# Kernel tuning notes

Hardware: AMD Instinct MI355X
Metric: run time of the kernel (lower is better)

The kernel has to match this reference:

```python
import jax, jax.numpy as jnp
import numpy as np

B, S, P = 2, 1024, 1024          # batch, new tokens, start_pos (cached prefix)
E, H, KV, HD = 2048, 32, 8, 64    # embed, heads, kv groups, head_dim
G = H // KV                       # group size = 4
THETA = 500000.0
CTX = P + S                       # cache/context length = 2048


def _rope_tables(start, seqlen):
    inv_freq = 1.0 / (THETA ** (jnp.arange(0, HD, 2, dtype=jnp.float32) / HD))
    pos = jnp.arange(start, start + seqlen, dtype=jnp.float32)
    freqs = jnp.outer(pos, inv_freq)              # [S, HD/2]
    emb = jnp.concatenate([freqs, freqs], axis=-1)  # [S, HD]
    return jnp.cos(emb), jnp.sin(emb)


def setup_inputs() -> dict:
    key = jax.random.key(0)
    ks = jax.random.split(key, 8)
    x = jax.random.normal(ks[0], (B, S, E), dtype=jnp.float32)
    cos1, sin1 = _rope_tables(P, S)
    cos = jnp.broadcast_to(cos1[None], (B, S, HD))
    sin = jnp.broadcast_to(sin1[None], (B, S, HD))
    # causal-with-offset additive mask: query i (global pos P+i) sees key j <= P+i
    qpos = P + jnp.arange(S)[:, None]
    kpos = jnp.arange(CTX)[None, :]
    mask = jnp.where(kpos <= qpos, 0.0, -1e9).astype(jnp.float32)[None, None]  # [1,1,S,CTX]
    cache_k = jax.random.normal(ks[1], (B, KV, CTX, HD), dtype=jnp.float32)
    cache_v = jax.random.normal(ks[2], (B, KV, CTX, HD), dtype=jnp.float32)
    sc = 0.02
    Wq = jax.random.normal(ks[3], (E, E), dtype=jnp.float32) * sc
    Wk = jax.random.normal(ks[4], (KV * HD, E), dtype=jnp.float32) * sc
    Wv = jax.random.normal(ks[5], (KV * HD, E), dtype=jnp.float32) * sc
    Wo = jax.random.normal(ks[6], (E, E), dtype=jnp.float32) * sc
    return {"x": x, "cos": cos, "sin": sin, "mask": mask,
            "cache_k": cache_k, "cache_v": cache_v,
            "Wq": Wq, "Wk": Wk, "Wv": Wv, "Wo": Wo, "start_pos": P}


def _rotate_half(t):
    t1, t2 = t[..., : HD // 2], t[..., HD // 2:]
    return jnp.concatenate([-t2, t1], axis=-1)


def _apply_rope(t, cos, sin):
    # t: [B, nh, S, HD]; cos/sin: [B, S, HD] -> unsqueeze head dim
    c = cos[:, None]
    s = sin[:, None]
    return t * c + _rotate_half(t) * s


def reference(x, cos, sin, mask, cache_k, cache_v, Wq, Wk, Wv, Wo, start_pos):
    b, s, e = x.shape
    q = (x @ Wq.T).reshape(b, s, H, HD).transpose(0, 2, 1, 3)    # [B,H,S,HD]
    k = (x @ Wk.T).reshape(b, s, KV, HD).transpose(0, 2, 1, 3)   # [B,KV,S,HD]
    v = (x @ Wv.T).reshape(b, s, KV, HD).transpose(0, 2, 1, 3)
    q = _apply_rope(q, cos, sin)
    k = _apply_rope(k, cos, sin)
    ck = cache_k.at[:, :, start_pos:start_pos + s].set(k)
    cv = cache_v.at[:, :, start_pos:start_pos + s].set(v)
    keys = ck[:, :, : start_pos + s]      # [B,KV,T,HD]
    vals = cv[:, :, : start_pos + s]
    # GQA without materializing repeated KV: view q as [B,KV,G,S,HD]
    qg = q.reshape(b, KV, G, s, HD)
    scores = jnp.einsum("bkgsh,bkth->bkgst", qg, keys) / jnp.sqrt(jnp.float32(HD))
    scores = scores + mask[:, :, None]    # broadcast mask over group dim
    probs = jax.nn.softmax(scores.astype(jnp.float32), axis=-1).astype(x.dtype)
    out = jnp.einsum("bkgst,bkth->bkgsh", probs, vals)            # [B,KV,G,S,HD]
    out = out.reshape(b, H, s, HD).transpose(0, 2, 1, 3).reshape(b, s, e)
    return out @ Wo.T
```

## Files before the change

kernel.cpp:

```cpp
#include <hip/hip_runtime.h>
#include <cstddef>

#define B   2
#define S   1024
#define PP  1024
#define CTX 2048
#define E   2048
#define H   32
#define KVH 8
#define HD  64
#define GQ  4
#define NQKV 3072

typedef short s4v  __attribute__((ext_vector_type(4)));
typedef short s8v  __attribute__((ext_vector_type(8)));
typedef float f4v  __attribute__((ext_vector_type(4)));

__device__ __forceinline__ short f2bf(float f) {
  union { float f; unsigned u; } v; v.f = f;
  unsigned r = v.u + 0x7fffu + ((v.u >> 16) & 1u);
  return (short)(r >> 16);
}
__device__ __forceinline__ float bf2f(short h) {
  union { unsigned u; float f; } v; v.u = ((unsigned)(unsigned short)h) << 16;
  return v.f;
}

__device__ __forceinline__ void gl_lds16(const void* g, void* l) {
  __builtin_amdgcn_global_load_lds((const __attribute__((address_space(1))) unsigned*)g,
                                   (__attribute__((address_space(3))) unsigned*)l, 16, 0, 0);
}

__global__ __launch_bounds__(256) void prep(const float* __restrict__ x,
                                            const float* __restrict__ Wq,
                                            const float* __restrict__ Wk,
                                            const float* __restrict__ Wv,
                                            short* __restrict__ xb,
                                            short* __restrict__ wqkv) {
  const int blk = blockIdx.x, tid = threadIdx.x;
  const float* s; short* d; int base;
  if (blk < 2048)      { s = x;  d = xb;             base = blk; }
  else if (blk < 4096) { s = Wq; d = wqkv;           base = blk - 2048; }
  else if (blk < 4608) { s = Wk; d = wqkv + 4194304; base = blk - 4096; }
  else                 { s = Wv; d = wqkv + 5242880; base = blk - 4608; }
  int i = (base * 256 + tid) * 8;
  float4 a = *(const float4*)&s[i];
  float4 b = *(const float4*)&s[i + 4];
  s8v o;
  o[0]=f2bf(a.x); o[1]=f2bf(a.y); o[2]=f2bf(a.z); o[3]=f2bf(a.w);
  o[4]=f2bf(b.x); o[5]=f2bf(b.y); o[6]=f2bf(b.z); o[7]=f2bf(b.w);
  *(s8v*)&d[i] = o;
}

__global__ __launch_bounds__(256) void qkv_gemm(const short* __restrict__ A,
                                                const short* __restrict__ Bw,
                                                const float* __restrict__ cosb,
                                                const float* __restrict__ sinb,
                                                const float* __restrict__ Wo,
                                                const float* __restrict__ ck,
                                                const float* __restrict__ cv,
                                                short* __restrict__ qb,
                                                short* __restrict__ keys,
                                                short* __restrict__ vt,
                                                short* __restrict__ wob,
                                                float4* __restrict__ outz) {
  __shared__ short As[2][8192];
  __shared__ short Bs[2][8192];
  const int tid = threadIdx.x;
  const int id  = blockIdx.x;

  if (id >= 384) {
    const int aux = id - 384;
    if (aux < 2048) {
      int i = (aux * 256 + tid) * 8;
      float4 a = *(const float4*)&Wo[i];
      float4 b = *(const float4*)&Wo[i + 4];
      s8v o;
      o[0]=f2bf(a.x); o[1]=f2bf(a.y); o[2]=f2bf(a.z); o[3]=f2bf(a.w);
      o[4]=f2bf(b.x); o[5]=f2bf(b.y); o[6]=f2bf(b.z); o[7]=f2bf(b.w);
      *(s8v*)&wob[i] = o;
    } else if (aux < 2560) {
      int idx = (aux - 2048) * 256 + tid;
      int bkv = idx >> 13;
      int rem = idx & 8191;
      size_t off = (size_t)bkv * (CTX * HD) + (size_t)rem * 8;
      float4 a = *(const float4*)&ck[off];
      float4 b = *(const float4*)&ck[off + 4];
      s8v o;
      o[0]=f2bf(a.x); o[1]=f2bf(a.y); o[2]=f2bf(a.z); o[3]=f2bf(a.w);
      o[4]=f2bf(b.x); o[5]=f2bf(b.y); o[6]=f2bf(b.z); o[7]=f2bf(b.w);
      *(s8v*)&keys[off] = o;
    } else if (aux < 2816) {
      short (*Ts)[72] = (short (*)[72])&As[0][0];
      const int blk2 = aux - 2560;
      const int bkv = blk2 >> 4;
      const int p0  = (blk2 & 15) * 64;
      const float* src = cv + (size_t)bkv * CTX * HD + (size_t)p0 * HD;
      {
        int dq = tid & 15, kb = tid >> 4;
        float4 vv[4];
#pragma unroll
        for (int i = 0; i < 4; i++)
          vv[i] = *(const float4*)&src[(size_t)(kb * 4 + i) * HD + dq * 4];
#pragma unroll
        for (int j = 0; j < 4; j++) {
          s4v p;
          p[0]=f2bf(((const float*)&vv[0])[j]); p[1]=f2bf(((const float*)&vv[1])[j]);
          p[2]=f2bf(((const float*)&vv[2])[j]); p[3]=f2bf(((const float*)&vv[3])[j]);
          *(s4v*)&Ts[dq * 4 + j][kb * 4] = p;
        }
      }
      __syncthreads();
      {
        int d = tid >> 2, c = tid & 3;
        short* dst = vt + ((size_t)bkv * HD + d) * CTX + p0 + (c >> 1) * 32 + (c & 1) * 4;
#pragma unroll
        for (int j = 0; j < 4; j++) {
          s4v q4 = *(const s4v*)&Ts[d][c * 16 + j * 4];
          *(s4v*)&dst[j * 8] = q4;
        }
      }
    } else {
      int i0 = (aux - 2816) * 1024 + tid * 4;
#pragma unroll
      for (int j = 0; j < 4; j++) outz[i0 + j] = make_float4(0.f, 0.f, 0.f, 0.f);
    }
    return;
  }

  const int wv   = tid >> 6, lane = tid & 63;
  const int wm   = wv & 1, wn = wv >> 1;
  const int n16  = lane & 15, g = lane >> 4;
  const int m0   = (id / 24) * 128, n0 = (id % 24) * 128;
  const int K = 2048;

  const int rr = tid >> 3;
  const int cc = ((tid & 7) ^ (rr & 7)) * 8;
  const short* pA = A  + (size_t)(m0 + rr) * K + cc;
  const short* pB = Bw + (size_t)(n0 + rr) * K + cc;

  auto stage = [&](int buf, int kofs) {
#pragma unroll
    for (int st = 0; st < 4; st++) {
      gl_lds16(pA + kofs + (size_t)st * 32 * K, &As[buf][(st * 256 + wv * 64) * 8]);
      gl_lds16(pB + kofs + (size_t)st * 32 * K, &Bs[buf][(st * 256 + wv * 64) * 8]);
    }
  };

  f4v acc[4][4] = {};
  stage(0, 0);
  int cur = 0;
  for (int k0 = 0; k0 < K; k0 += 64) {
    __syncthreads();
    if (k0 + 64 < K) stage(cur ^ 1, k0 + 64);

#pragma unroll
    for (int kk = 0; kk < 2; kk++) {
      s8v af[4], bf[4];
#pragma unroll
      for (int mt = 0; mt < 4; mt++)
        af[mt] = *(const s8v*)&As[cur][(wm * 64 + mt * 16 + n16) * 64 + (((kk << 2) | g) ^ (n16 & 7)) * 8];
#pragma unroll
      for (int nt = 0; nt < 4; nt++)
        bf[nt] = *(const s8v*)&Bs[cur][(wn * 64 + nt * 16 + n16) * 64 + (((kk << 2) | g) ^ (n16 & 7)) * 8];
#pragma unroll
      for (int mt = 0; mt < 4; mt++)
#pragma unroll
        for (int nt = 0; nt < 4; nt++)
          acc[mt][nt] = __builtin_amdgcn_mfma_f32_16x16x32_bf16(af[mt], bf[nt], acc[mt][nt], 0, 0, 0);
    }
    cur ^= 1;
  }

  const int rowb = m0 + wm * 64 + g * 4;
  const int colb = n0 + wn * 64 + n16;
  if (n0 < 2048) {
#pragma unroll
    for (int mt = 0; mt < 4; mt++)
#pragma unroll
      for (int nt = 0; nt < 4; nt++) {
        size_t base = (size_t)(rowb + mt * 16) * E + colb + nt * 16;
#pragma unroll
        for (int r = 0; r < 4; r++)
          qb[base + (size_t)r * E] = f2bf(acc[mt][nt][r]);
      }
  } else if (n0 < 2560) {
    const int kvh = ((n0 - 2048) >> 6) + wn;
#pragma unroll
    for (int mt = 0; mt < 4; mt++) {
      const int row = rowb + mt * 16;
      const int bb = row >> 10, s = row & 1023;
      const float* crow = cosb + ((size_t)bb * S + s) * HD;
      const float* srow = sinb + ((size_t)bb * S + s) * HD;
      const size_t kdst = (((size_t)bb * KVH + kvh) * CTX + PP + s) * HD;
#pragma unroll
      for (int nt = 0; nt < 2; nt++) {
        const int d = n16 + nt * 16;
#pragma unroll
        for (int r = 0; r < 4; r++) {
          float c  = crow[r * HD + d];
          float sn = srow[r * HD + d];
          float k1 = acc[mt][nt][r], k2 = acc[mt][nt + 2][r];
          keys[kdst + (size_t)r * HD + d]      = f2bf(k1 * c - k2 * sn);
          keys[kdst + (size_t)r * HD + d + 32] = f2bf(k2 * c + k1 * sn);
        }
      }
    }
  } else {
    const int b    = m0 >> 10;
    const int head = ((n0 - 2560) >> 6) + wn;
    const int sbase = (m0 - (b << 10)) + wm * 64;
    const size_t vrowb = (size_t)(b * KVH + head) * HD;
#pragma unroll
    for (int mt = 0; mt < 4; mt++) {
      const int pos = PP + sbase + ((mt >> 1) << 5) + ((mt & 1) << 2) + (g << 3);
#pragma unroll
      for (int nt = 0; nt < 4; nt++) {
        const int d = nt * 16 + n16;
        s4v o;
        o[0] = f2bf(acc[mt][nt][0]); o[1] = f2bf(acc[mt][nt][1]);
        o[2] = f2bf(acc[mt][nt][2]); o[3] = f2bf(acc[mt][nt][3]);
        *(s4v*)&vt[(vrowb + d) * CTX + pos] = o;
      }
    }
  }
}

__global__ __launch_bounds__(256) void gemm_bf16_sk(const short* __restrict__ A,
                                                    const short* __restrict__ Bw,
                                                    float* __restrict__ C,
                                                    int M, int N, int K) {
  __shared__ short As[2][8192];
  __shared__ short Bs[2][8192];
  const int tid  = threadIdx.x;
  const int wv   = tid >> 6, lane = tid & 63;
  const int wm   = wv & 1, wn = wv >> 1;
  const int n16  = lane & 15, g = lane >> 4;
  const int m0   = blockIdx.y * 128, n0 = blockIdx.x * 128;
  const int kh   = K >> 1;
  const int kbeg = blockIdx.z * kh;

  const int rr = tid >> 3;
  const int cc = ((tid & 7) ^ (rr & 7)) * 8;
  const short* pA = A  + (size_t)(m0 + rr) * K + kbeg + cc;
  const short* pB = Bw + (size_t)(n0 + rr) * K + kbeg + cc;

  auto stage = [&](int buf, int kofs) {
#pragma unroll
    for (int st = 0; st < 4; st++) {
      gl_lds16(pA + kofs + (size_t)st * 32 * K, &As[buf][(st * 256 + wv * 64) * 8]);
      gl_lds16(pB + kofs + (size_t)st * 32 * K, &Bs[buf][(st * 256 + wv * 64) * 8]);
    }
  };

  f4v acc[4][4] = {};
  stage(0, 0);
  int cur = 0;
  for (int k0 = 0; k0 < kh; k0 += 64) {
    __syncthreads();
    if (k0 + 64 < kh) stage(cur ^ 1, k0 + 64);

#pragma unroll
    for (int kk = 0; kk < 2; kk++) {
      s8v af[4], bf[4];
#pragma unroll
      for (int mt = 0; mt < 4; mt++)
        af[mt] = *(const s8v*)&As[cur][(wm * 64 + mt * 16 + n16) * 64 + (((kk << 2) | g) ^ (n16 & 7)) * 8];
#pragma unroll
      for (int nt = 0; nt < 4; nt++)
        bf[nt] = *(const s8v*)&Bs[cur][(wn * 64 + nt * 16 + n16) * 64 + (((kk << 2) | g) ^ (n16 & 7)) * 8];
#pragma unroll
      for (int mt = 0; mt < 4; mt++)
#pragma unroll
        for (int nt = 0; nt < 4; nt++)
          acc[mt][nt] = __builtin_amdgcn_mfma_f32_16x16x32_bf16(af[mt], bf[nt], acc[mt][nt], 0, 0, 0);
    }
    cur ^= 1;
  }

#pragma unroll
  for (int mt = 0; mt < 4; mt++)
#pragma unroll
    for (int nt = 0; nt < 4; nt++) {
      size_t base = (size_t)(m0 + wm * 64 + mt * 16 + g * 4) * N + n0 + wn * 64 + nt * 16 + n16;
#pragma unroll
      for (int r = 0; r < 4; r++)
        unsafeAtomicAdd(&C[base + (size_t)r * N], acc[mt][nt][r]);
    }
}

__global__ __launch_bounds__(256) void attn_mfma(const short* __restrict__ qb,
                                                 const float* __restrict__ cosb,
                                                 const float* __restrict__ sinb,
                                                 const short* __restrict__ keys,
                                                 const short* __restrict__ valsT,
                                                 short* __restrict__ attn) {
  __shared__ short Ks[4096];
  __shared__ short VTs[4096];

  const int sblk = 15 - (blockIdx.x & 15);
  const int h    = (blockIdx.x >> 4) & (H - 1);
  const int b    = blockIdx.x >> 9;
  const int kv   = h >> 2;
  const int sq0  = sblk * 64;
  const int kend = PP + sq0 + 64;

  const int tid  = threadIdx.x;
  const int w    = tid >> 6;
  const int lane = tid & 63;
  const int n    = lane & 15;
  const int g    = lane >> 4;

  const short* kbase = keys  + ((size_t)b * KVH + kv) * CTX * HD;
  const short* vtb   = valsT + ((size_t)b * KVH + kv) * (size_t)HD * CTX;

  union { s4v h4[2]; s8v v; } qlo, qhi;
  {
    const size_t row = (size_t)b * S + sq0 + w * 16 + n;
    const short* qrow = qb + row * E + h * 64;
    const float* crow = cosb + row * HD;
    const float* srow = sinb + row * HD;
    const float SC = 0.18033688011112042f;
    s8v q0 = *(const s8v*)&qrow[g * 8];
    s8v q1 = *(const s8v*)&qrow[32 + g * 8];
    float cc[8], ss[8];
    *(float4*)&cc[0] = *(const float4*)&crow[g * 8];
    *(float4*)&cc[4] = *(const float4*)&crow[g * 8 + 4];
    *(float4*)&ss[0] = *(const float4*)&srow[g * 8];
    *(float4*)&ss[4] = *(const float4*)&srow[g * 8 + 4];
#pragma unroll
    for (int j = 0; j < 8; j++) {
      float fl = bf2f(q0[j]), fh = bf2f(q1[j]);
      qlo.v[j] = f2bf((fl * cc[j] - fh * ss[j]) * SC);
      qhi.v[j] = f2bf((fh * cc[j] + fl * ss[j]) * SC);
    }
  }

  f4v O[4] = {{0,0,0,0},{0,0,0,0},{0,0,0,0},{0,0,0,0}};
  float la[4] = {0.f, 0.f, 0.f, 0.f};
  const int qp     = PP + sq0 + w * 16 + n;
  const int qmin_w = PP + sq0 + w * 16;

  const int lrow = lane >> 3;
  const int sw   = (lane & 7) ^ lrow;
  const short* kg0 = kbase + (size_t)(w * 8 + lrow) * HD + sw * 8;
  const short* kg1 = kg0 + 32 * HD;
  const short* vg0 = vtb + (size_t)(w * 8 + lrow) * CTX + sw * 8;
  const short* vg1 = vg0 + (size_t)32 * CTX;
  short* kl0 = Ks + w * 512;
  short* kl1 = Ks + 2048 + w * 512;
  short* vl0 = VTs + w * 512;
  short* vl1 = VTs + 2048 + w * 512;

  const int xsl = (g ^ (n & 7)) * 8;

  for (int k0 = 0; k0 < kend; k0 += 64) {
    __syncthreads();
    gl_lds16(kg0 + (size_t)k0 * HD, kl0);
    gl_lds16(kg1 + (size_t)k0 * HD, kl1);
    gl_lds16(vg0 + k0, vl0);
    gl_lds16(vg1 + k0, vl1);
    __syncthreads();

    if (k0 >= qmin_w + 16) continue;

    f4v sc[4];
    __builtin_amdgcn_s_setprio(1);
#pragma unroll
    for (int st = 0; st < 4; st++) {
      const short* krow = &Ks[(st * 16 + n) * 64];
      s8v alo = *(const s8v*)(krow + xsl);
      s8v ahi = *(const s8v*)(krow + (xsl ^ 32));
      f4v z = {0.f, 0.f, 0.f, 0.f};
      z = __builtin_amdgcn_mfma_f32_16x16x32_bf16(alo, qlo.v, z, 0, 0, 0);
      sc[st] = __builtin_amdgcn_mfma_f32_16x16x32_bf16(ahi, qhi.v, z, 0, 0, 0);
    }
    __builtin_amdgcn_s_setprio(0);

    if (k0 + 63 > qmin_w) {
#pragma unroll
      for (int st = 0; st < 4; st++)
#pragma unroll
        for (int r = 0; r < 4; r++) {
          int kpos = k0 + st * 16 + g * 4 + r;
          if (kpos > qp) sc[st][r] = -3e38f;
        }
    }

    union { unsigned u[4]; s8v v; } pb0, pb1;
#pragma unroll
    for (int st = 0; st < 4; st++) {
      float e0 = __builtin_amdgcn_exp2f(sc[st][0]);
      float e1 = __builtin_amdgcn_exp2f(sc[st][1]);
      float e2 = __builtin_amdgcn_exp2f(sc[st][2]);
      float e3 = __builtin_amdgcn_exp2f(sc[st][3]);
      la[0] += e0; la[1] += e1; la[2] += e2; la[3] += e3;
      unsigned w0, w1;
      asm("v_cvt_pk_bf16_f32 %0, %1, %2" : "=v"(w0) : "v"(e0), "v"(e1));
      asm("v_cvt_pk_bf16_f32 %0, %1, %2" : "=v"(w1) : "v"(e2), "v"(e3));
      if (st < 2) { pb0.u[st * 2] = w0; pb0.u[st * 2 + 1] = w1; }
      else        { pb1.u[(st - 2) * 2] = w0; pb1.u[(st - 2) * 2 + 1] = w1; }
    }

    __builtin_amdgcn_s_setprio(1);
#pragma unroll
    for (int dg = 0; dg < 4; dg++) {
      const short* vr = &VTs[(dg * 16 + n) * 64];
      s8v va = *(const s8v*)(vr + xsl);
      s8v vx = *(const s8v*)(vr + (xsl ^ 32));
      O[dg] = __builtin_amdgcn_mfma_f32_16x16x32_bf16(va, pb0.v, O[dg], 0, 0, 0);
      O[dg] = __builtin_amdgcn_mfma_f32_16x16x32_bf16(vx, pb1.v, O[dg], 0, 0, 0);
    }
    __builtin_amdgcn_s_setprio(0);
  }

  float l = (la[0] + la[1]) + (la[2] + la[3]);
  l += __shfl_xor(l, 16);
  l += __shfl_xor(l, 32);
  const float rl = 1.f / l;
  short* orow = attn + ((size_t)b * S + sq0 + w * 16 + n) * E + h * 64;
#pragma unroll
  for (int dg = 0; dg < 4; dg++) {
    s4v o;
    o[0] = f2bf(O[dg][0] * rl); o[1] = f2bf(O[dg][1] * rl);
    o[2] = f2bf(O[dg][2] * rl); o[3] = f2bf(O[dg][3] * rl);
    *(s4v*)&orow[dg * 16 + g * 4] = o;
  }
}

extern "C" void kernel_launch(void* const* d_in, const int* in_sizes, int n_in,
                              void* d_out, int out_size, void* d_ws, size_t ws_size,
                              hipStream_t stream) {
  const float* x       = (const float*)d_in[0];
  const float* cosb    = (const float*)d_in[1];
  const float* sinb    = (const float*)d_in[2];
  const float* cache_k = (const float*)d_in[4];
  const float* cache_v = (const float*)d_in[5];
  const float* Wq      = (const float*)d_in[6];
  const float* Wk      = (const float*)d_in[7];
  const float* Wv      = (const float*)d_in[8];
  const float* Wo      = (const float*)d_in[9];
  float* out = (float*)d_out;

  short* xb    = (short*)d_ws;
  short* wqkv  = xb + 4194304;
  short* wob   = wqkv + 6291456;
  short* keysb = wob + 4194304;
  short* valsT = keysb + 2097152;
  short* aout  = valsT + 2097152;
  short* qb    = aout + 4194304;

  dim3 blk(256);

  prep<<<5120, blk, 0, stream>>>(x, Wq, Wk, Wv, xb, wqkv);

  qkv_gemm<<<4224, blk, 0, stream>>>(xb, wqkv, cosb, sinb, Wo, cache_k, cache_v,
                                     qb, keysb, valsT, wob, (float4*)out);

  attn_mfma<<<B * H * (S / 64), blk, 0, stream>>>(qb, cosb, sinb, keysb, valsT, aout);

  gemm_bf16_sk<<<dim3(E / 128, (B * S) / 128, 2), blk, 0, stream>>>(aout, wob, out, B * S, E, E);
}
```

Before: 253.0 us.

## Use 2-wave attention blocks with 32 query rows per wave; memset output

The attention kernel now runs 128 threads per block, and each wave handles two 16-row query groups instead of one. Each K/V fragment read from LDS is therefore reused for twice as many MFMAs, and each wave loads four K/V chunks per tile. Output zeroing for the split-K GEMM moves out of the qkv_gemm auxiliary blocks into a hipMemsetAsync, which shrinks that grid. The cost is higher register pressure from doubled accumulators and fewer waves per block to hide latency.

```diff
diff --git a/kernel.cpp b/kernel.cpp
--- a/kernel.cpp
+++ b/kernel.cpp
@@ -62,8 +62,7 @@
                                                 short* __restrict__ qb,
                                                 short* __restrict__ keys,
                                                 short* __restrict__ vt,
-                                                short* __restrict__ wob,
-                                                float4* __restrict__ outz) {
+                                                short* __restrict__ wob) {
   __shared__ short As[2][8192];
   __shared__ short Bs[2][8192];
   const int tid = threadIdx.x;
@@ -90,7 +89,7 @@
       o[0]=f2bf(a.x); o[1]=f2bf(a.y); o[2]=f2bf(a.z); o[3]=f2bf(a.w);
       o[4]=f2bf(b.x); o[5]=f2bf(b.y); o[6]=f2bf(b.z); o[7]=f2bf(b.w);
       *(s8v*)&keys[off] = o;
-    } else if (aux < 2816) {
+    } else {
       short (*Ts)[72] = (short (*)[72])&As[0][0];
       const int blk2 = aux - 2560;
       const int bkv = blk2 >> 4;
@@ -120,10 +119,6 @@
           *(s4v*)&dst[j * 8] = q4;
         }
       }
-    } else {
-      int i0 = (aux - 2816) * 1024 + tid * 4;
-#pragma unroll
-      for (int j = 0; j < 4; j++) outz[i0 + j] = make_float4(0.f, 0.f, 0.f, 0.f);
     }
     return;
   }
@@ -289,7 +284,7 @@
     }
 }
 
-__global__ __launch_bounds__(256) void attn_mfma(const short* __restrict__ qb,
+__global__ __launch_bounds__(128) void attn_mfma(const short* __restrict__ qb,
                                                  const float* __restrict__ cosb,
                                                  const float* __restrict__ sinb,
                                                  const short* __restrict__ keys,
@@ -314,9 +309,10 @@
   const short* kbase = keys  + ((size_t)b * KVH + kv) * CTX * HD;
   const short* vtb   = valsT + ((size_t)b * KVH + kv) * (size_t)HD * CTX;
 
-  union { s4v h4[2]; s8v v; } qlo, qhi;
-  {
-    const size_t row = (size_t)b * S + sq0 + w * 16 + n;
+  s8v qlo[2], qhi[2];
+#pragma unroll
+  for (int qg = 0; qg < 2; qg++) {
+    const size_t row = (size_t)b * S + sq0 + w * 32 + qg * 16 + n;
     const short* qrow = qb + row * E + h * 64;
     const float* crow = cosb + row * HD;
     const float* srow = sinb + row * HD;
@@ -331,75 +327,81 @@
 #pragma unroll
     for (int j = 0; j < 8; j++) {
       float fl = bf2f(q0[j]), fh = bf2f(q1[j]);
-      qlo.v[j] = f2bf((fl * cc[j] - fh * ss[j]) * SC);
-      qhi.v[j] = f2bf((fh * cc[j] + fl * ss[j]) * SC);
-    }
-  }
-
-  f4v O[4] = {{0,0,0,0},{0,0,0,0},{0,0,0,0},{0,0,0,0}};
-  float la[4] = {0.f, 0.f, 0.f, 0.f};
-  const int qp     = PP + sq0 + w * 16 + n;
-  const int qmin_w = PP + sq0 + w * 16;
+      qlo[qg][j] = f2bf((fl * cc[j] - fh * ss[j]) * SC);
+      qhi[qg][j] = f2bf((fh * cc[j] + fl * ss[j]) * SC);
+    }
+  }
+
+  f4v O[2][4] = {};
+  float la[2][4] = {};
+  const int qmin_w = PP + sq0 + w * 32;
 
   const int lrow = lane >> 3;
   const int sw   = (lane & 7) ^ lrow;
-  const short* kg0 = kbase + (size_t)(w * 8 + lrow) * HD + sw * 8;
-  const short* kg1 = kg0 + 32 * HD;
-  const short* vg0 = vtb + (size_t)(w * 8 + lrow) * CTX + sw * 8;
-  const short* vg1 = vg0 + (size_t)32 * CTX;
-  short* kl0 = Ks + w * 512;
-  short* kl1 = Ks + 2048 + w * 512;
-  short* vl0 = VTs + w * 512;
-  short* vl1 = VTs + 2048 + w * 512;
+  const short* kg = kbase + (size_t)(w * 32 + lrow) * HD + sw * 8;
+  const short* vg = vtb + (size_t)(w * 32 + lrow) * CTX + sw * 8;
+  short* const kl = Ks  + (w * 32) * 64;
+  short* const vl = VTs + (w * 32) * 64;
 
   const int xsl = (g ^ (n & 7)) * 8;
 
   for (int k0 = 0; k0 < kend; k0 += 64) {
     __syncthreads();
-    gl_lds16(kg0 + (size_t)k0 * HD, kl0);
-    gl_lds16(kg1 + (size_t)k0 * HD, kl1);
-    gl_lds16(vg0 + k0, vl0);
-    gl_lds16(vg1 + k0, vl1);
+#pragma unroll
+    for (int j = 0; j < 4; j++) {
+      gl_lds16(kg + (size_t)(k0 + j * 8) * HD, kl + j * 512);
+      gl_lds16(vg + (size_t)(j * 8) * CTX + k0, vl + j * 512);
+    }
     __syncthreads();
 
-    if (k0 >= qmin_w + 16) continue;
-
-    f4v sc[4];
+    if (k0 >= qmin_w + 32) continue;
+
+    f4v sc[2][4];
     __builtin_amdgcn_s_setprio(1);
 #pragma unroll
     for (int st = 0; st < 4; st++) {
       const short* krow = &Ks[(st * 16 + n) * 64];
       s8v alo = *(const s8v*)(krow + xsl);
       s8v ahi = *(const s8v*)(krow + (xsl ^ 32));
-      f4v z = {0.f, 0.f, 0.f, 0.f};
-      z = __builtin_amdgcn_mfma_f32_16x16x32_bf16(alo, qlo.v, z, 0, 0, 0);
-      sc[st] = __builtin_amdgcn_mfma_f32_16x16x32_bf16(ahi, qhi.v, z, 0, 0, 0);
+#pragma unroll
+      for (int qg = 0; qg < 2; qg++) {
+        f4v z = {0.f, 0.f, 0.f, 0.f};
+        z = __builtin_amdgcn_mfma_f32_16x16x32_bf16(alo, qlo[qg], z, 0, 0, 0);
+        sc[qg][st] = __builtin_amdgcn_mfma_f32_16x16x32_bf16(ahi, qhi[qg], z, 0, 0, 0);
+      }
     }
     __builtin_amdgcn_s_setprio(0);
 
     if (k0 + 63 > qmin_w) {
 #pragma unroll
-      for (int st = 0; st < 4; st++)
-#pragma unroll
-        for (int r = 0; r < 4; r++) {
-          int kpos = k0 + st * 16 + g * 4 + r;
-          if (kpos > qp) sc[st][r] = -3e38f;
-        }
-    }
-
-    union { unsigned u[4]; s8v v; } pb0, pb1;
-#pragma unroll
-    for (int st = 0; st < 4; st++) {
-      float e0 = __builtin_amdgcn_exp2f(sc[st][0]);
-      float e1 = __builtin_amdgcn_exp2f(sc[st][1]);
-      float e2 = __builtin_amdgcn_exp2f(sc[st][2]);
-      float e3 = __builtin_amdgcn_exp2f(sc[st][3]);
-      la[0] += e0; la[1] += e1; la[2] += e2; la[3] += e3;
-      unsigned w0, w1;
-      asm("v_cvt_pk_bf16_f32 %0, %1, %2" : "=v"(w0) : "v"(e0), "v"(e1));
-      asm("v_cvt_pk_bf16_f32 %0, %1, %2" : "=v"(w1) : "v"(e2), "v"(e3));
-      if (st < 2) { pb0.u[st * 2] = w0; pb0.u[st * 2 + 1] = w1; }
-      else        { pb1.u[(st - 2) * 2] = w0; pb1.u[(st - 2) * 2 + 1] = w1; }
+      for (int qg = 0; qg < 2; qg++) {
+        const int qp = qmin_w + qg * 16 + n;
+#pragma unroll
+        for (int st = 0; st < 4; st++)
+#pragma unroll
+          for (int r = 0; r < 4; r++) {
+            int kpos = k0 + st * 16 + g * 4 + r;
+            if (kpos > qp) sc[qg][st][r] = -3e38f;
+          }
+      }
+    }
+
+    union pu { unsigned u[4]; s8v v; } pb0[2], pb1[2];
+#pragma unroll
+    for (int qg = 0; qg < 2; qg++) {
+#pragma unroll
+      for (int st = 0; st < 4; st++) {
+        float e0 = __builtin_amdgcn_exp2f(sc[qg][st][0]);
+        float e1 = __builtin_amdgcn_exp2f(sc[qg][st][1]);
+        float e2 = __builtin_amdgcn_exp2f(sc[qg][st][2]);
+        float e3 = __builtin_amdgcn_exp2f(sc[qg][st][3]);
+        la[qg][0] += e0; la[qg][1] += e1; la[qg][2] += e2; la[qg][3] += e3;
+        unsigned w0, w1;
+        asm("v_cvt_pk_bf16_f32 %0, %1, %2" : "=v"(w0) : "v"(e0), "v"(e1));
+        asm("v_cvt_pk_bf16_f32 %0, %1, %2" : "=v"(w1) : "v"(e2), "v"(e3));
+        if (st < 2) { pb0[qg].u[st * 2] = w0; pb0[qg].u[st * 2 + 1] = w1; }
+        else        { pb1[qg].u[(st - 2) * 2] = w0; pb1[qg].u[(st - 2) * 2 + 1] = w1; }
+      }
     }
 
     __builtin_amdgcn_s_setprio(1);
@@ -408,23 +410,29 @@
       const short* vr = &VTs[(dg * 16 + n) * 64];
       s8v va = *(const s8v*)(vr + xsl);
       s8v vx = *(const s8v*)(vr + (xsl ^ 32));
-      O[dg] = __builtin_amdgcn_mfma_f32_16x16x32_bf16(va, pb0.v, O[dg], 0, 0, 0);
-      O[dg] = __builtin_amdgcn_mfma_f32_16x16x32_bf16(vx, pb1.v, O[dg], 0, 0, 0);
+#pragma unroll
+      for (int qg = 0; qg < 2; qg++) {
+        O[qg][dg] = __builtin_amdgcn_mfma_f32_16x16x32_bf16(va, pb0[qg].v, O[qg][dg], 0, 0, 0);
+        O[qg][dg] = __builtin_amdgcn_mfma_f32_16x16x32_bf16(vx, pb1[qg].v, O[qg][dg], 0, 0, 0);
+      }
     }
     __builtin_amdgcn_s_setprio(0);
   }
 
-  float l = (la[0] + la[1]) + (la[2] + la[3]);
-  l += __shfl_xor(l, 16);
-  l += __shfl_xor(l, 32);
-  const float rl = 1.f / l;
-  short* orow = attn + ((size_t)b * S + sq0 + w * 16 + n) * E + h * 64;
-#pragma unroll
-  for (int dg = 0; dg < 4; dg++) {
-    s4v o;
-    o[0] = f2bf(O[dg][0] * rl); o[1] = f2bf(O[dg][1] * rl);
-    o[2] = f2bf(O[dg][2] * rl); o[3] = f2bf(O[dg][3] * rl);
-    *(s4v*)&orow[dg * 16 + g * 4] = o;
+#pragma unroll
+  for (int qg = 0; qg < 2; qg++) {
+    float l = (la[qg][0] + la[qg][1]) + (la[qg][2] + la[qg][3]);
+    l += __shfl_xor(l, 16);
+    l += __shfl_xor(l, 32);
+    const float rl = 1.f / l;
+    short* orow = attn + ((size_t)b * S + sq0 + w * 32 + qg * 16 + n) * E + h * 64;
+#pragma unroll
+    for (int dg = 0; dg < 4; dg++) {
+      s4v o;
+      o[0] = f2bf(O[qg][dg][0] * rl); o[1] = f2bf(O[qg][dg][1] * rl);
+      o[2] = f2bf(O[qg][dg][2] * rl); o[3] = f2bf(O[qg][dg][3] * rl);
+      *(s4v*)&orow[dg * 16 + g * 4] = o;
+    }
   }
 }
 
@@ -452,12 +460,14 @@
 
   dim3 blk(256);
 
+  hipMemsetAsync(out, 0, (size_t)out_size, stream);
+
   prep<<<5120, blk, 0, stream>>>(x, Wq, Wk, Wv, xb, wqkv);
 
-  qkv_gemm<<<4224, blk, 0, stream>>>(xb, wqkv, cosb, sinb, Wo, cache_k, cache_v,
-                                     qb, keysb, valsT, wob, (float4*)out);
-
-  attn_mfma<<<B * H * (S / 64), blk, 0, stream>>>(qb, cosb, sinb, keysb, valsT, aout);
+  qkv_gemm<<<3200, blk, 0, stream>>>(xb, wqkv, cosb, sinb, Wo, cache_k, cache_v,
+                                     qb, keysb, valsT, wob);
+
+  attn_mfma<<<B * H * (S / 64), dim3(128), 0, stream>>>(qb, cosb, sinb, keysb, valsT, aout);
 
   gemm_bf16_sk<<<dim3(E / 128, (B * S) / 128, 2), blk, 0, stream>>>(aout, wob, out, B * S, E, E);
 }
```

Result: slower. 263.8 us (+4.3%).
